# Kernel optimization log

Hardware: AMD Instinct MI355X
Metric: run time of the kernel (lower is better)

The kernel has to match this reference:

```python
import jax, jax.numpy as jnp
import numpy as np
import math

D_MODEL = 1024
D_STATE = 16
D_CONV = 4
EXPAND = 2
D_INNER = EXPAND * D_MODEL
DT_RANK = math.ceil(D_MODEL / 16)
EPS = 1e-5


def setup_inputs() -> dict:
    key = jax.random.key(0)
    ks = jax.random.split(key, 8)
    B, L = 2, 1024
    s = 0.02
    return {
        "hidden_states": jax.random.normal(ks[0], (B, L, D_MODEL), jnp.float32),
        "norm_weight": jnp.ones((D_MODEL,), jnp.float32),
        "in_proj_w": (jax.random.normal(ks[1], (2 * D_INNER, D_MODEL), jnp.float32) * s),
        "conv_w": (jax.random.normal(ks[2], (D_INNER, D_CONV), jnp.float32) * s),
        "conv_b": jnp.zeros((D_INNER,), jnp.float32),
        "x_proj_w": (jax.random.normal(ks[3], (DT_RANK + 2 * D_STATE, D_INNER), jnp.float32) * s),
        "dt_proj_w": (jax.random.normal(ks[4], (D_INNER, DT_RANK), jnp.float32) * s),
        "dt_proj_b": jax.random.uniform(ks[5], (D_INNER,), jnp.float32, -4.0, -2.0),
        "A_log": jnp.log(jnp.broadcast_to(jnp.arange(1, D_STATE + 1, dtype=jnp.float32), (D_INNER, D_STATE))),
        "D": jnp.ones((D_INNER,), jnp.float32),
        "out_proj_w": (jax.random.normal(ks[6], (D_MODEL, D_INNER), jnp.float32) * s),
    }


def _rmsnorm(x, w):
    # Faithful to source: rms = ||x||_2 / sqrt(d); x / (rms + eps) * w
    norm = jnp.linalg.norm(x, axis=-1, keepdims=True)
    rms = norm * (1.0 / math.sqrt(x.shape[-1]))
    return w * (x / (rms + EPS))


def _mamba(h, in_proj_w, conv_w, conv_b, x_proj_w, dt_proj_w, dt_proj_b, A_log, D, out_proj_w):
    B, L, _ = h.shape
    xz = h @ in_proj_w.T                      # (B,L,2*D_INNER)
    x, z = jnp.split(xz, 2, axis=-1)          # each (B,L,D_INNER)

    # causal depthwise conv1d along L, kernel D_CONV
    xpad = jnp.pad(x, ((0, 0), (D_CONV - 1, 0), (0, 0)))
    xc = conv_b
    for k in range(D_CONV):                   # tiny fixed loop over kernel taps
        xc = xc + xpad[:, k:k + L, :] * conv_w[:, k]
    xc = jax.nn.silu(xc)                      # (B,L,D_INNER)

    x_dbl = xc @ x_proj_w.T                   # (B,L,DT_RANK+2N)
    dt, Bm, Cm = jnp.split(x_dbl, [DT_RANK, DT_RANK + D_STATE], axis=-1)
    dt = jax.nn.softplus(dt @ dt_proj_w.T + dt_proj_b)   # (B,L,D_INNER)

    A = -jnp.exp(A_log)                       # (D_INNER,N)
    deltaA = jnp.exp(dt[..., None] * A)                      # (B,L,D_INNER,N)
    deltaBu = (dt * xc)[..., None] * Bm[:, :, None, :]        # (B,L,D_INNER,N)

    def step(hst, inp):
        dA, dBu, Ct = inp
        hst = dA * hst + dBu                  # (B,D_INNER,N)
        y = jnp.einsum('bdn,bn->bd', hst, Ct)
        return hst, y

    h0 = jnp.zeros((B, D_INNER, D_STATE), xc.dtype)
    _, ys = jax.lax.scan(step, h0, (deltaA.swapaxes(0, 1), deltaBu.swapaxes(0, 1), Cm.swapaxes(0, 1)))
    y = ys.swapaxes(0, 1)                     # (B,L,D_INNER)
    y = y + D * xc
    y = y * jax.nn.silu(z)
    return y @ out_proj_w.T                   # (B,L,D_MODEL)


def reference(hidden_states, norm_weight, in_proj_w, conv_w, conv_b, x_proj_w,
              dt_proj_w, dt_proj_b, A_log, D, out_proj_w):
    residual = hidden_states
    h = _rmsnorm(residual, norm_weight)
    out = _mamba(h, in_proj_w, conv_w, conv_b, x_proj_w, dt_proj_w, dt_proj_b,
                 A_log, D, out_proj_w)
    return out, residual
```

## Files before the change

kernel.cpp:

```cpp
#include <hip/hip_runtime.h>

typedef __bf16 bf16x8 __attribute__((ext_vector_type(8)));
typedef float f32x4 __attribute__((ext_vector_type(4)));

__device__ __forceinline__ float b2f(ushort u) {
    union { unsigned int i; float f; } v;
    v.i = ((unsigned int)u) << 16;
    return v.f;
}
__device__ __forceinline__ ushort f2b(float f) {
    union { float f; unsigned int i; } v;
    v.f = f;
    unsigned int x = v.i;
    unsigned int r = (x + 0x7fffu + ((x >> 16) & 1u)) >> 16;
    return (ushort)r;
}
__device__ __forceinline__ float fexp2(float x) {
#if __has_builtin(__builtin_amdgcn_exp2f)
    return __builtin_amdgcn_exp2f(x);
#else
    return exp2f(x);
#endif
}
__device__ __forceinline__ void gload16(const ushort* g, ushort* l) {
    __builtin_amdgcn_global_load_lds(
        (const __attribute__((address_space(1))) unsigned int*)g,
        (__attribute__((address_space(3))) unsigned int*)l, 16, 0, 0);
}
__device__ __forceinline__ bf16x8 ldsfrag(const ushort* s, int row, int cq) {
    int p = cq ^ (row & 7);
    return *(const bf16x8*)(s + row * 64 + p * 8);
}

#define D_MODEL 1024
#define D_INNER 2048
#define D_STATE 16
#define DT_RANK 64
#define NTOK    2048
#define LSEQ    1024
#define NCH     64
#define LC      16
#define KSL     16
#define LOG2E   1.44269504088896f

__global__ __launch_bounds__(256) void prep_kernel(
    const float* __restrict__ hs, const float* __restrict__ w,
    ushort* __restrict__ hout, float* __restrict__ resid,
    const float* __restrict__ inproj, const float* __restrict__ outproj,
    const float* __restrict__ xprojw, const float* __restrict__ dtw,
    ushort* __restrict__ wIn, ushort* __restrict__ wOut,
    ushort* __restrict__ xpw, ushort* __restrict__ dtwb,
    float* __restrict__ xdbl)
{
    int blk = blockIdx.x;
    int tid = threadIdx.x;
    if (blk < NTOK) {
        int t = blk;
        float4 r4 = *(const float4*)(hs + (size_t)t * D_MODEL + tid * 4);
        float s = r4.x * r4.x + r4.y * r4.y + r4.z * r4.z + r4.w * r4.w;
        #pragma unroll
        for (int off = 32; off >= 1; off >>= 1) s += __shfl_xor(s, off);
        __shared__ float red[4];
        int lane = tid & 63, wid = tid >> 6;
        if (lane == 0) red[wid] = s;
        __syncthreads();
        float tot = red[0] + red[1] + red[2] + red[3];
        float inv = 1.0f / (sqrtf(tot) * (1.0f / 32.0f) + 1e-5f);
        float4 w4 = *(const float4*)(w + tid * 4);
        ushort4 o;
        o.x = f2b(w4.x * r4.x * inv);
        o.y = f2b(w4.y * r4.y * inv);
        o.z = f2b(w4.z * r4.z * inv);
        o.w = f2b(w4.w * r4.w * inv);
        *(ushort4*)(hout + (size_t)t * D_MODEL + tid * 4) = o;
        *(float4*)(resid + (size_t)t * D_MODEL + tid * 4) = r4;
    } else if (blk < NTOK + 6464) {
        int i = (blk - NTOK) * 256 + tid;
        const float* src; ushort* dst; int off;
        if (i < 1048576)      { src = inproj;  dst = wIn;  off = i; }
        else if (i < 1572864) { src = outproj; dst = wOut; off = i - 1048576; }
        else if (i < 1622016) { src = xprojw;  dst = xpw;  off = i - 1572864; }
        else if (i < 1654784) { src = dtw;     dst = dtwb; off = i - 1622016; }
        else return;
        float4 v = *(const float4*)(src + (size_t)off * 4);
        ushort4 o;
        o.x = f2b(v.x); o.y = f2b(v.y); o.z = f2b(v.z); o.w = f2b(v.w);
        *(ushort4*)(dst + (size_t)off * 4) = o;
    } else {
        int i = (blk - NTOK - 6464) * 256 + tid;
        if (i < 49152)
            *(float4*)(xdbl + (size_t)i * 4) = (float4){0.f, 0.f, 0.f, 0.f};
    }
}

__global__ __launch_bounds__(256) void gemm_xz_kernel(
    const ushort* __restrict__ Ag, const ushort* __restrict__ Wg,
    ushort* __restrict__ xq, ushort* __restrict__ zq, int K)
{
    __shared__ __align__(16) ushort sA[128 * 64];
    __shared__ __align__(16) ushort sB[128 * 64];
    int tid = threadIdx.x;
    int bm = blockIdx.x, bn = blockIdx.y;
    int wid = tid >> 6, lane = tid & 63;
    int wm = (wid >> 1) * 64, wn = (wid & 1) * 64;
    int l16 = lane & 15, q = lane >> 4;

    f32x4 acc[4][4];
    #pragma unroll
    for (int i = 0; i < 4; i++)
        #pragma unroll
        for (int j = 0; j < 4; j++)
            acc[i][j] = (f32x4){0.f, 0.f, 0.f, 0.f};

    const ushort* Abase = Ag + (size_t)bm * 128 * K;
    const ushort* Wbase = Wg + (size_t)bn * 128 * K;

    int segr = lane >> 3, segc = lane & 7;
    size_t goff[4]; int sseg[4];
    #pragma unroll
    for (int t = 0; t < 4; t++) {
        int s = wid * 4 + t;
        int r = s * 8 + segr;
        int gc = segc ^ (r & 7);
        sseg[t] = s * 512;
        goff[t] = (size_t)r * K + gc * 8;
    }

    for (int k0 = 0; k0 < K; k0 += 64) {
        __syncthreads();
        #pragma unroll
        for (int t = 0; t < 4; t++) {
            gload16(Abase + goff[t] + k0, sA + sseg[t]);
            gload16(Wbase + goff[t] + k0, sB + sseg[t]);
        }
        __syncthreads();
        #pragma unroll
        for (int ks = 0; ks < 2; ks++) {
            int cq = ks * 4 + q;
            bf16x8 af[4], bfr[4];
            #pragma unroll
            for (int i = 0; i < 4; i++)
                af[i] = ldsfrag(sA, wm + i * 16 + l16, cq);
            #pragma unroll
            for (int j = 0; j < 4; j++)
                bfr[j] = ldsfrag(sB, wn + j * 16 + l16, cq);
            #pragma unroll
            for (int i = 0; i < 4; i++)
                #pragma unroll
                for (int j = 0; j < 4; j++)
                    acc[i][j] = __builtin_amdgcn_mfma_f32_16x16x32_bf16(af[i], bfr[j], acc[i][j], 0, 0, 0);
        }
    }

    ushort* dst = (bn < 16) ? xq : zq;
    int row0 = bm * 128 + wm + q * 4;
    int col0 = (bn & 15) * 128 + wn + l16;
    #pragma unroll
    for (int i = 0; i < 4; i++)
        #pragma unroll
        for (int j = 0; j < 4; j++)
            #pragma unroll
            for (int r = 0; r < 4; r++)
                dst[(size_t)(row0 + i * 16 + r) * D_INNER + col0 + j * 16] =
                    f2b(acc[i][j][r]);
}

__global__ __launch_bounds__(256) void gemm64_kernel(
    const ushort* __restrict__ Ag, const ushort* __restrict__ Wg,
    float* __restrict__ Cf, int M, int N, int K)
{
    __shared__ __align__(16) ushort sA[64 * 64];
    __shared__ __align__(16) ushort sB[64 * 64];
    int tid = threadIdx.x;
    int bm = blockIdx.x, bn = blockIdx.y;
    int wid = tid >> 6, lane = tid & 63;
    int wm = wid * 16;
    int l16 = lane & 15, q = lane >> 4;

    f32x4 acc[4];
    #pragma unroll
    for (int j = 0; j < 4; j++) acc[j] = (f32x4){0.f, 0.f, 0.f, 0.f};

    const ushort* Abase = Ag + (size_t)bm * 64 * K;
    const ushort* Wbase = Wg + (size_t)bn * 64 * K;

    int segr = lane >> 3, segc = lane & 7;
    size_t goff[2]; int sseg[2];
    #pragma unroll
    for (int t = 0; t < 2; t++) {
        int s = wid * 2 + t;
        int r = s * 8 + segr;
        int gc = segc ^ (r & 7);
        sseg[t] = s * 512;
        goff[t] = (size_t)r * K + gc * 8;
    }

    for (int k0 = 0; k0 < K; k0 += 64) {
        __syncthreads();
        #pragma unroll
        for (int t = 0; t < 2; t++) {
            gload16(Abase + goff[t] + k0, sA + sseg[t]);
            gload16(Wbase + goff[t] + k0, sB + sseg[t]);
        }
        __syncthreads();
        #pragma unroll
        for (int ks = 0; ks < 2; ks++) {
            int cq = ks * 4 + q;
            bf16x8 af = ldsfrag(sA, wm + l16, cq);
            bf16x8 bfr[4];
            #pragma unroll
            for (int j = 0; j < 4; j++)
                bfr[j] = ldsfrag(sB, j * 16 + l16, cq);
            #pragma unroll
            for (int j = 0; j < 4; j++)
                acc[j] = __builtin_amdgcn_mfma_f32_16x16x32_bf16(af, bfr[j], acc[j], 0, 0, 0);
        }
    }

    int row0 = bm * 64 + wm + q * 4;
    int col0 = bn * 64 + l16;
    #pragma unroll
    for (int j = 0; j < 4; j++)
        #pragma unroll
        for (int r = 0; r < 4; r++)
            Cf[(size_t)(row0 + r) * N + col0 + j * 16] = acc[j][r];
}

__global__ __launch_bounds__(256) void conv_silu_kernel(
    const ushort* __restrict__ xq, const float* __restrict__ cw,
    const float* __restrict__ cb, ushort* __restrict__ xcb)
{
    int idx = blockIdx.x * 256 + threadIdx.x;
    int d = idx & (D_INNER - 1);
    int t = idx >> 11;
    int l = t & (LSEQ - 1), b = t >> 10;
    float4 w4 = *(const float4*)(cw + d * 4);
    float acc = cb[d];
    float wk[4] = {w4.x, w4.y, w4.z, w4.w};
    #pragma unroll
    for (int k = 0; k < 4; k++) {
        int ll = l - 3 + k;
        float xv = (ll >= 0) ? b2f(xq[(((size_t)(b * LSEQ + ll)) << 11) + d]) : 0.f;
        acc += xv * wk[k];
    }
    float sg = acc / (1.f + __expf(-acc));
    xcb[idx] = f2b(sg);
}

__global__ __launch_bounds__(256) void xproj_partial_kernel(
    const ushort* __restrict__ xcb, const ushort* __restrict__ wq,
    float* __restrict__ xdbl)
{
    __shared__ __align__(16) ushort sA[128 * 32];
    __shared__ __align__(16) ushort sB[96 * 32];
    int tid = threadIdx.x;
    int bm = blockIdx.x, sl = blockIdx.y;
    int wid = tid >> 6, lane = tid & 63;
    int wm = wid * 32;
    int l16 = lane & 15, q = lane >> 4;

    f32x4 acc[2][6];
    #pragma unroll
    for (int i = 0; i < 2; i++)
        #pragma unroll
        for (int j = 0; j < 6; j++)
            acc[i][j] = (f32x4){0.f, 0.f, 0.f, 0.f};

    const ushort* Abase = xcb + (size_t)bm * 128 * D_INNER;
    int kbase = sl * (D_INNER / KSL);

    for (int kk = 0; kk < D_INNER / KSL; kk += 32) {
        int k0 = kbase + kk;
        __syncthreads();
        #pragma unroll
        for (int i = tid; i < 512; i += 256) {
            int r = i >> 2, c = (i & 3) << 3;
            *(uint4*)(sA + i * 8) = *(const uint4*)(Abase + (size_t)r * D_INNER + k0 + c);
        }
        for (int i = tid; i < 384; i += 256) {
            int r = i >> 2, c = (i & 3) << 3;
            *(uint4*)(sB + i * 8) = *(const uint4*)(wq + (size_t)r * D_INNER + k0 + c);
        }
        __syncthreads();
        bf16x8 af[2], bfr[6];
        #pragma unroll
        for (int i = 0; i < 2; i++)
            af[i] = *(const bf16x8*)(sA + (wm + i * 16 + l16) * 32 + q * 8);
        #pragma unroll
        for (int j = 0; j < 6; j++)
            bfr[j] = *(const bf16x8*)(sB + (j * 16 + l16) * 32 + q * 8);
        #pragma unroll
        for (int i = 0; i < 2; i++)
            #pragma unroll
            for (int j = 0; j < 6; j++)
                acc[i][j] = __builtin_amdgcn_mfma_f32_16x16x32_bf16(af[i], bfr[j], acc[i][j], 0, 0, 0);
    }

    int row0 = bm * 128 + wm + q * 4;
    #pragma unroll
    for (int i = 0; i < 2; i++)
        #pragma unroll
        for (int j = 0; j < 6; j++)
            #pragma unroll
            for (int r = 0; r < 4; r++)
                atomicAdd(&xdbl[(size_t)(row0 + i * 16 + r) * 96 + j * 16 + l16],
                          acc[i][j][r]);
}

__global__ __launch_bounds__(256) void dt_gemm_kernel(
    const float* __restrict__ xdbl, const ushort* __restrict__ dtwq,
    const float* __restrict__ dtb, ushort* __restrict__ dtout)
{
    __shared__ __align__(16) ushort sA[64 * 72];
    __shared__ __align__(16) ushort sB[64 * 72];
    int tid = threadIdx.x;
    int bm = blockIdx.x, bn = blockIdx.y;
    int wid = tid >> 6, lane = tid & 63;
    int wm = wid * 16;
    int l16 = lane & 15, q = lane >> 4;

    const float* Abase = xdbl + (size_t)bm * 64 * 96;
    const ushort* Bbase = dtwq + (size_t)bn * 64 * DT_RANK;
    #pragma unroll
    for (int i = tid; i < 512; i += 256) {
        int r = i >> 3, c = (i & 7) << 3;
        float4 v0 = *(const float4*)(Abase + (size_t)r * 96 + c);
        float4 v1 = *(const float4*)(Abase + (size_t)r * 96 + c + 4);
        ushort o[8] = {f2b(v0.x), f2b(v0.y), f2b(v0.z), f2b(v0.w),
                       f2b(v1.x), f2b(v1.y), f2b(v1.z), f2b(v1.w)};
        *(uint4*)(sA + r * 72 + c) = *(const uint4*)o;
        *(uint4*)(sB + r * 72 + c) = *(const uint4*)(Bbase + (size_t)r * DT_RANK + c);
    }
    __syncthreads();

    f32x4 acc[4];
    #pragma unroll
    for (int j = 0; j < 4; j++) acc[j] = (f32x4){0.f, 0.f, 0.f, 0.f};

    #pragma unroll
    for (int ks = 0; ks < 2; ks++) {
        bf16x8 af = *(const bf16x8*)(sA + (wm + l16) * 72 + ks * 32 + q * 8);
        bf16x8 bfr[4];
        #pragma unroll
        for (int j = 0; j < 4; j++)
            bfr[j] = *(const bf16x8*)(sB + (j * 16 + l16) * 72 + ks * 32 + q * 8);
        #pragma unroll
        for (int j = 0; j < 4; j++)
            acc[j] = __builtin_amdgcn_mfma_f32_16x16x32_bf16(af, bfr[j], acc[j], 0, 0, 0);
    }

    __syncthreads();
    #pragma unroll
    for (int j = 0; j < 4; j++) {
        float bias = dtb[bn * 64 + j * 16 + l16];
        #pragma unroll
        for (int r = 0; r < 4; r++) {
            float s = acc[j][r] + bias;
            float sp = (s > 20.f) ? s : log1pf(__expf(s));
            sA[(wm + q * 4 + r) * 72 + j * 16 + l16] = f2b(sp);
        }
    }
    __syncthreads();
    int row0 = bm * 64, col0 = bn * 64;
    #pragma unroll
    for (int rep = 0; rep < 2; rep++) {
        int off = rep * 2048 + tid * 8;
        int row = off >> 6, col = off & 63;
        *(uint4*)(dtout + (size_t)(row0 + row) * D_INNER + col0 + col) =
            *(const uint4*)(sA + row * 72 + col);
    }
}

__global__ __launch_bounds__(256) void scan_partA_kernel(
    const ushort* __restrict__ dt, const ushort* __restrict__ xcq,
    const float* __restrict__ xdbl, const float* __restrict__ Alog,
    float2* __restrict__ ch)
{
    __shared__ float sBC[LC][32];
    int bid = blockIdx.x;
    int g = bid & 7;
    int c = (bid >> 3) & (NCH - 1);
    int b = bid >> 9;
    int tid = threadIdx.x;
    int lane = tid & 63, wid = tid >> 6;
    int d = g * 256 + wid * 64 + lane;
    int l0 = c * LC;

    if (tid < LC * 8) {
        int r = tid >> 3, c4 = (tid & 7) * 4;
        *(float4*)&sBC[r][c4] =
            *(const float4*)(xdbl + ((size_t)(b * LSEQ + l0 + r)) * 96 + 64 + c4);
    }
    float A[16];
    #pragma unroll
    for (int k = 0; k < 4; k++)
        *(float4*)&A[k * 4] = *(const float4*)(Alog + d * D_STATE + k * 4);
    #pragma unroll
    for (int n = 0; n < 16; n++) A[n] = -__expf(A[n]) * LOG2E;
    __syncthreads();

    const ushort* dtp = dt  + ((size_t)(b * LSEQ + l0)) * D_INNER + d;
    const ushort* xcp = xcq + ((size_t)(b * LSEQ + l0)) * D_INNER + d;

    float h[16], ap[16];
    #pragma unroll
    for (int n = 0; n < 16; n++) { h[n] = 0.f; ap[n] = 1.f; }

    for (int l = 0; l < LC; l++) {
        float dtv = b2f(dtp[(size_t)l * D_INNER]);
        float xcv = b2f(xcp[(size_t)l * D_INNER]);
        float t = dtv * xcv;
        float Bv[16];
        #pragma unroll
        for (int k = 0; k < 4; k++)
            *(float4*)&Bv[k * 4] = *(const float4*)&sBC[l][k * 4];
        #pragma unroll
        for (int n = 0; n < 16; n++) {
            float a = fexp2(dtv * A[n]);
            h[n] = h[n] * a + t * Bv[n];
            ap[n] *= a;
        }
    }

    float2* outp = ch + (((size_t)(c * 2 + b)) << 15) + (d << 4);
    #pragma unroll
    for (int n = 0; n < 16; n += 2) {
        float4 v = {ap[n], h[n], ap[n + 1], h[n + 1]};
        *(float4*)&outp[n] = v;
    }
}

__global__ __launch_bounds__(256) void scan_partB_kernel(float2* __restrict__ ch)
{
    int kk = blockIdx.x * 256 + threadIdx.x;
    int b = kk >> 15, dn = kk & 32767;
    float run = 0.f;
    #pragma unroll 8
    for (int c = 0; c < NCH; c++) {
        float2* p = ch + (((size_t)(c * 2 + b)) << 15) + dn;
        float2 v = *p;
        p->x = run;
        run = v.x * run + v.y;
    }
}

__global__ __launch_bounds__(256) void scan_partC_kernel(
    const ushort* __restrict__ dt, const ushort* __restrict__ xcq,
    const float* __restrict__ xdbl, const ushort* __restrict__ zq,
    const float* __restrict__ Alog, const float* __restrict__ Dp,
    const float2* __restrict__ ch, ushort* __restrict__ yg)
{
    __shared__ float sBC[LC][32];
    int bid = blockIdx.x;
    int g = bid & 7;
    int c = (bid >> 3) & (NCH - 1);
    int b = bid >> 9;
    int tid = threadIdx.x;
    int lane = tid & 63, wid = tid >> 6;
    int d = g * 256 + wid * 64 + lane;
    int l0 = c * LC;

    if (tid < LC * 8) {
        int r = tid >> 3, c4 = (tid & 7) * 4;
        *(float4*)&sBC[r][c4] =
            *(const float4*)(xdbl + ((size_t)(b * LSEQ + l0 + r)) * 96 + 64 + c4);
    }
    float A[16];
    #pragma unroll
    for (int k = 0; k < 4; k++)
        *(float4*)&A[k * 4] = *(const float4*)(Alog + d * D_STATE + k * 4);
    #pragma unroll
    for (int n = 0; n < 16; n++) A[n] = -__expf(A[n]) * LOG2E;
    float Dd = Dp[d];

    const float2* hip_ = ch + (((size_t)(c * 2 + b)) << 15) + (d << 4);
    float h[16];
    #pragma unroll
    for (int n = 0; n < 16; n += 2) {
        float4 v = *(const float4*)&hip_[n];
        h[n] = v.x; h[n + 1] = v.z;
    }
    __syncthreads();

    const ushort* dtp = dt  + ((size_t)(b * LSEQ + l0)) * D_INNER + d;
    const ushort* xcp = xcq + ((size_t)(b * LSEQ + l0)) * D_INNER + d;
    const ushort* zp  = zq  + ((size_t)(b * LSEQ + l0)) * D_INNER + d;
    ushort* yp = yg + ((size_t)(b * LSEQ + l0)) * D_INNER + d;

    for (int l = 0; l < LC; l++) {
        float dtv = b2f(dtp[(size_t)l * D_INNER]);
        float xcv = b2f(xcp[(size_t)l * D_INNER]);
        float zv  = b2f(zp[(size_t)l * D_INNER]);
        float t = dtv * xcv;
        float Bv[16], Cv[16];
        #pragma unroll
        for (int k = 0; k < 4; k++) {
            *(float4*)&Bv[k * 4] = *(const float4*)&sBC[l][k * 4];
            *(float4*)&Cv[k * 4] = *(const float4*)&sBC[l][16 + k * 4];
        }
        float p0 = 0.f, p1 = 0.f, p2 = 0.f, p3 = 0.f;
        #pragma unroll
        for (int n = 0; n < 16; n += 4) {
            float a0 = fexp2(dtv * A[n]);
            float a1 = fexp2(dtv * A[n + 1]);
            float a2 = fexp2(dtv * A[n + 2]);
            float a3 = fexp2(dtv * A[n + 3]);
            h[n]     = h[n] * a0 + t * Bv[n];
            h[n + 1] = h[n + 1] * a1 + t * Bv[n + 1];
            h[n + 2] = h[n + 2] * a2 + t * Bv[n + 2];
            h[n + 3] = h[n + 3] * a3 + t * Bv[n + 3];
            p0 += h[n] * Cv[n];
            p1 += h[n + 1] * Cv[n + 1];
            p2 += h[n + 2] * Cv[n + 2];
            p3 += h[n + 3] * Cv[n + 3];
        }
        float p = (p0 + p1) + (p2 + p3);
        float y = p + Dd * xcv;
        float sz = zv / (1.f + __expf(-zv));
        yp[(size_t)l * D_INNER] = f2b(y * sz);
    }
}

extern "C" void kernel_launch(void* const* d_in, const int* in_sizes, int n_in,
                              void* d_out, int out_size, void* d_ws, size_t ws_size,
                              hipStream_t stream)
{
    const float* hs      = (const float*)d_in[0];
    const float* norm_w  = (const float*)d_in[1];
    const float* inproj  = (const float*)d_in[2];
    const float* convw   = (const float*)d_in[3];
    const float* convb   = (const float*)d_in[4];
    const float* xprojw  = (const float*)d_in[5];
    const float* dtw     = (const float*)d_in[6];
    const float* dtb     = (const float*)d_in[7];
    const float* alog    = (const float*)d_in[8];
    const float* dvec    = (const float*)d_in[9];
    const float* outproj = (const float*)d_in[10];

    float* out_main  = (float*)d_out;
    float* out_resid = (float*)d_out + (size_t)NTOK * D_MODEL;

    char* ws = (char*)d_ws;
    ushort* xq      = (ushort*)(ws);
    ushort* zq      = (ushort*)(ws +  8388608);
    ushort* dtq     = (ushort*)(ws + 16777216);
    ushort* xcb     = (ushort*)(ws + 25165824);
    float2* ch      = (float2*)(ws + 33554432);
    float*  xdbl    = (float*) (ws + 67108864);
    ushort* wIn     = (ushort*)(ws + 67895296);
    ushort* wOut    = (ushort*)(ws + 76283904);
    ushort* h_bf16  = (ushort*)(ws + 80478208);
    ushort* xpw_b   = (ushort*)(ws + 84672512);
    ushort* dtw_b   = (ushort*)(ws + 85065728);
    ushort* yg_bf16 = (ushort*)(ws + 85327872);

    prep_kernel<<<NTOK + 6464 + 192, 256, 0, stream>>>(
        hs, norm_w, h_bf16, out_resid,
        inproj, outproj, xprojw, dtw, wIn, wOut, xpw_b, dtw_b, xdbl);

    gemm_xz_kernel<<<dim3(NTOK / 128, (2 * D_INNER) / 128), 256, 0, stream>>>(
        h_bf16, wIn, xq, zq, D_MODEL);

    conv_silu_kernel<<<(NTOK * D_INNER) / 256, 256, 0, stream>>>(
        xq, convw, convb, xcb);

    xproj_partial_kernel<<<dim3(NTOK / 128, KSL), 256, 0, stream>>>(
        xcb, xpw_b, xdbl);

    dt_gemm_kernel<<<dim3(NTOK / 64, D_INNER / 64), 256, 0, stream>>>(
        xdbl, dtw_b, dtb, dtq);

    scan_partA_kernel<<<1024, 256, 0, stream>>>(dtq, xcb, xdbl, alog, ch);
    scan_partB_kernel<<<256, 256, 0, stream>>>(ch);
    scan_partC_kernel<<<1024, 256, 0, stream>>>(dtq, xcb, xdbl, zq,
                                                alog, dvec, ch, yg_bf16);

    gemm64_kernel<<<dim3(NTOK / 64, D_MODEL / 64), 256, 0, stream>>>(
        yg_bf16, wOut, out_main, NTOK, D_MODEL, D_INNER);
}
```

Baseline: 254.5 us.

## Retile out-proj GEMM with split-K atomics, vectorize conv, enlarge scan chunks

The output projection moves from 64x64 tiles to 128x128 tiles with a two-way K split that accumulates into a pre-zeroed output using float atomics. The zeroing is added to the prep kernel. Separately, the conv+SiLU kernel is vectorized to eight channels per thread, and the x_proj shared-memory tiles are padded to avoid bank conflicts. The scan chunk count is halved with longer chunks, the chunk-state pass now writes initial states to a separate float buffer, and the scan loops are unrolled. Atomics add non-determinism and extra traffic, and fewer scan blocks lowers parallelism.

```diff
diff --git a/kernel.cpp b/kernel.cpp
--- a/kernel.cpp
+++ b/kernel.cpp
@@ -38,8 +38,8 @@
 #define DT_RANK 64
 #define NTOK    2048
 #define LSEQ    1024
-#define NCH     64
-#define LC      16
+#define NCH     32
+#define LC      32
 #define KSL     16
 #define LOG2E   1.44269504088896f
 
@@ -50,7 +50,7 @@
     const float* __restrict__ xprojw, const float* __restrict__ dtw,
     ushort* __restrict__ wIn, ushort* __restrict__ wOut,
     ushort* __restrict__ xpw, ushort* __restrict__ dtwb,
-    float* __restrict__ xdbl)
+    float* __restrict__ xdbl, float* __restrict__ outz)
 {
     int blk = blockIdx.x;
     int tid = threadIdx.x;
@@ -86,10 +86,14 @@
         ushort4 o;
         o.x = f2b(v.x); o.y = f2b(v.y); o.z = f2b(v.z); o.w = f2b(v.w);
         *(ushort4*)(dst + (size_t)off * 4) = o;
-    } else {
+    } else if (blk < NTOK + 6464 + 192) {
         int i = (blk - NTOK - 6464) * 256 + tid;
         if (i < 49152)
             *(float4*)(xdbl + (size_t)i * 4) = (float4){0.f, 0.f, 0.f, 0.f};
+    } else {
+        int i = (blk - NTOK - 6464 - 192) * 256 + tid;
+        if (i < 524288)
+            *(float4*)(outz + (size_t)i * 4) = (float4){0.f, 0.f, 0.f, 0.f};
     }
 }
 
@@ -165,40 +169,45 @@
                     f2b(acc[i][j][r]);
 }
 
-__global__ __launch_bounds__(256) void gemm64_kernel(
+__global__ __launch_bounds__(256) void gemm_out_kernel(
     const ushort* __restrict__ Ag, const ushort* __restrict__ Wg,
-    float* __restrict__ Cf, int M, int N, int K)
-{
-    __shared__ __align__(16) ushort sA[64 * 64];
-    __shared__ __align__(16) ushort sB[64 * 64];
+    float* __restrict__ Cf)
+{
+    __shared__ __align__(16) ushort sA[128 * 64];
+    __shared__ __align__(16) ushort sB[128 * 64];
+    const int K = D_INNER;
     int tid = threadIdx.x;
-    int bm = blockIdx.x, bn = blockIdx.y;
+    int bm = blockIdx.x, bn = blockIdx.y, bz = blockIdx.z;
     int wid = tid >> 6, lane = tid & 63;
-    int wm = wid * 16;
+    int wm = (wid >> 1) * 64, wn = (wid & 1) * 64;
     int l16 = lane & 15, q = lane >> 4;
 
-    f32x4 acc[4];
-    #pragma unroll
-    for (int j = 0; j < 4; j++) acc[j] = (f32x4){0.f, 0.f, 0.f, 0.f};
-
-    const ushort* Abase = Ag + (size_t)bm * 64 * K;
-    const ushort* Wbase = Wg + (size_t)bn * 64 * K;
+    f32x4 acc[4][4];
+    #pragma unroll
+    for (int i = 0; i < 4; i++)
+        #pragma unroll
+        for (int j = 0; j < 4; j++)
+            acc[i][j] = (f32x4){0.f, 0.f, 0.f, 0.f};
+
+    const ushort* Abase = Ag + (size_t)bm * 128 * K;
+    const ushort* Wbase = Wg + (size_t)bn * 128 * K;
 
     int segr = lane >> 3, segc = lane & 7;
-    size_t goff[2]; int sseg[2];
-    #pragma unroll
-    for (int t = 0; t < 2; t++) {
-        int s = wid * 2 + t;
+    size_t goff[4]; int sseg[4];
+    #pragma unroll
+    for (int t = 0; t < 4; t++) {
+        int s = wid * 4 + t;
         int r = s * 8 + segr;
         int gc = segc ^ (r & 7);
         sseg[t] = s * 512;
         goff[t] = (size_t)r * K + gc * 8;
     }
 
-    for (int k0 = 0; k0 < K; k0 += 64) {
+    int kbeg = bz * (K / 2), kend = kbeg + K / 2;
+    for (int k0 = kbeg; k0 < kend; k0 += 64) {
         __syncthreads();
         #pragma unroll
-        for (int t = 0; t < 2; t++) {
+        for (int t = 0; t < 4; t++) {
             gload16(Abase + goff[t] + k0, sA + sseg[t]);
             gload16(Wbase + goff[t] + k0, sB + sseg[t]);
         }
@@ -206,53 +215,70 @@
         #pragma unroll
         for (int ks = 0; ks < 2; ks++) {
             int cq = ks * 4 + q;
-            bf16x8 af = ldsfrag(sA, wm + l16, cq);
-            bf16x8 bfr[4];
+            bf16x8 af[4], bfr[4];
+            #pragma unroll
+            for (int i = 0; i < 4; i++)
+                af[i] = ldsfrag(sA, wm + i * 16 + l16, cq);
             #pragma unroll
             for (int j = 0; j < 4; j++)
-                bfr[j] = ldsfrag(sB, j * 16 + l16, cq);
-            #pragma unroll
-            for (int j = 0; j < 4; j++)
-                acc[j] = __builtin_amdgcn_mfma_f32_16x16x32_bf16(af, bfr[j], acc[j], 0, 0, 0);
-        }
-    }
-
-    int row0 = bm * 64 + wm + q * 4;
-    int col0 = bn * 64 + l16;
-    #pragma unroll
-    for (int j = 0; j < 4; j++)
-        #pragma unroll
-        for (int r = 0; r < 4; r++)
-            Cf[(size_t)(row0 + r) * N + col0 + j * 16] = acc[j][r];
+                bfr[j] = ldsfrag(sB, wn + j * 16 + l16, cq);
+            #pragma unroll
+            for (int i = 0; i < 4; i++)
+                #pragma unroll
+                for (int j = 0; j < 4; j++)
+                    acc[i][j] = __builtin_amdgcn_mfma_f32_16x16x32_bf16(af[i], bfr[j], acc[i][j], 0, 0, 0);
+        }
+    }
+
+    int row0 = bm * 128 + wm + q * 4;
+    int col0 = bn * 128 + wn + l16;
+    #pragma unroll
+    for (int i = 0; i < 4; i++)
+        #pragma unroll
+        for (int j = 0; j < 4; j++)
+            #pragma unroll
+            for (int r = 0; r < 4; r++)
+                atomicAdd(&Cf[(size_t)(row0 + i * 16 + r) * D_MODEL + col0 + j * 16],
+                          acc[i][j][r]);
 }
 
 __global__ __launch_bounds__(256) void conv_silu_kernel(
     const ushort* __restrict__ xq, const float* __restrict__ cw,
     const float* __restrict__ cb, ushort* __restrict__ xcb)
 {
-    int idx = blockIdx.x * 256 + threadIdx.x;
-    int d = idx & (D_INNER - 1);
-    int t = idx >> 11;
+    int t = blockIdx.x;
+    int d0 = threadIdx.x * 8;
     int l = t & (LSEQ - 1), b = t >> 10;
-    float4 w4 = *(const float4*)(cw + d * 4);
-    float acc = cb[d];
-    float wk[4] = {w4.x, w4.y, w4.z, w4.w};
+
+    ushort v[4][8];
+    bool has[4];
     #pragma unroll
     for (int k = 0; k < 4; k++) {
         int ll = l - 3 + k;
-        float xv = (ll >= 0) ? b2f(xq[(((size_t)(b * LSEQ + ll)) << 11) + d]) : 0.f;
-        acc += xv * wk[k];
-    }
-    float sg = acc / (1.f + __expf(-acc));
-    xcb[idx] = f2b(sg);
+        has[k] = (ll >= 0);
+        if (has[k])
+            *(uint4*)v[k] = *(const uint4*)(xq + (((size_t)(b * LSEQ + ll)) << 11) + d0);
+    }
+    ushort o[8];
+    #pragma unroll
+    for (int j = 0; j < 8; j++) {
+        float4 w4 = *(const float4*)(cw + (size_t)(d0 + j) * 4);
+        float wk[4] = {w4.x, w4.y, w4.z, w4.w};
+        float acc = cb[d0 + j];
+        #pragma unroll
+        for (int k = 0; k < 4; k++)
+            if (has[k]) acc += b2f(v[k][j]) * wk[k];
+        o[j] = f2b(acc / (1.f + __expf(-acc)));
+    }
+    *(uint4*)(xcb + (((size_t)t) << 11) + d0) = *(const uint4*)o;
 }
 
 __global__ __launch_bounds__(256) void xproj_partial_kernel(
     const ushort* __restrict__ xcb, const ushort* __restrict__ wq,
     float* __restrict__ xdbl)
 {
-    __shared__ __align__(16) ushort sA[128 * 32];
-    __shared__ __align__(16) ushort sB[96 * 32];
+    __shared__ __align__(16) ushort sA[128 * 40];
+    __shared__ __align__(16) ushort sB[96 * 40];
     int tid = threadIdx.x;
     int bm = blockIdx.x, sl = blockIdx.y;
     int wid = tid >> 6, lane = tid & 63;
@@ -275,20 +301,20 @@
         #pragma unroll
         for (int i = tid; i < 512; i += 256) {
             int r = i >> 2, c = (i & 3) << 3;
-            *(uint4*)(sA + i * 8) = *(const uint4*)(Abase + (size_t)r * D_INNER + k0 + c);
+            *(uint4*)(sA + r * 40 + c) = *(const uint4*)(Abase + (size_t)r * D_INNER + k0 + c);
         }
         for (int i = tid; i < 384; i += 256) {
             int r = i >> 2, c = (i & 3) << 3;
-            *(uint4*)(sB + i * 8) = *(const uint4*)(wq + (size_t)r * D_INNER + k0 + c);
+            *(uint4*)(sB + r * 40 + c) = *(const uint4*)(wq + (size_t)r * D_INNER + k0 + c);
         }
         __syncthreads();
         bf16x8 af[2], bfr[6];
         #pragma unroll
         for (int i = 0; i < 2; i++)
-            af[i] = *(const bf16x8*)(sA + (wm + i * 16 + l16) * 32 + q * 8);
+            af[i] = *(const bf16x8*)(sA + (wm + i * 16 + l16) * 40 + q * 8);
         #pragma unroll
         for (int j = 0; j < 6; j++)
-            bfr[j] = *(const bf16x8*)(sB + (j * 16 + l16) * 32 + q * 8);
+            bfr[j] = *(const bf16x8*)(sB + (j * 16 + l16) * 40 + q * 8);
         #pragma unroll
         for (int i = 0; i < 2; i++)
             #pragma unroll
@@ -380,13 +406,13 @@
     int bid = blockIdx.x;
     int g = bid & 7;
     int c = (bid >> 3) & (NCH - 1);
-    int b = bid >> 9;
+    int b = bid >> 8;
     int tid = threadIdx.x;
     int lane = tid & 63, wid = tid >> 6;
     int d = g * 256 + wid * 64 + lane;
     int l0 = c * LC;
 
-    if (tid < LC * 8) {
+    {
         int r = tid >> 3, c4 = (tid & 7) * 4;
         *(float4*)&sBC[r][c4] =
             *(const float4*)(xdbl + ((size_t)(b * LSEQ + l0 + r)) * 96 + 64 + c4);
@@ -406,6 +432,7 @@
     #pragma unroll
     for (int n = 0; n < 16; n++) { h[n] = 0.f; ap[n] = 1.f; }
 
+    #pragma unroll 4
     for (int l = 0; l < LC; l++) {
         float dtv = b2f(dtp[(size_t)l * D_INNER]);
         float xcv = b2f(xcp[(size_t)l * D_INNER]);
@@ -430,16 +457,17 @@
     }
 }
 
-__global__ __launch_bounds__(256) void scan_partB_kernel(float2* __restrict__ ch)
+__global__ __launch_bounds__(256) void scan_partB_kernel(
+    const float2* __restrict__ ch, float* __restrict__ hinit)
 {
     int kk = blockIdx.x * 256 + threadIdx.x;
     int b = kk >> 15, dn = kk & 32767;
     float run = 0.f;
     #pragma unroll 8
     for (int c = 0; c < NCH; c++) {
-        float2* p = ch + (((size_t)(c * 2 + b)) << 15) + dn;
-        float2 v = *p;
-        p->x = run;
+        size_t off = (((size_t)(c * 2 + b)) << 15) + dn;
+        float2 v = ch[off];
+        hinit[off] = run;
         run = v.x * run + v.y;
     }
 }
@@ -448,19 +476,19 @@
     const ushort* __restrict__ dt, const ushort* __restrict__ xcq,
     const float* __restrict__ xdbl, const ushort* __restrict__ zq,
     const float* __restrict__ Alog, const float* __restrict__ Dp,
-    const float2* __restrict__ ch, ushort* __restrict__ yg)
+    const float* __restrict__ hinit, ushort* __restrict__ yg)
 {
     __shared__ float sBC[LC][32];
     int bid = blockIdx.x;
     int g = bid & 7;
     int c = (bid >> 3) & (NCH - 1);
-    int b = bid >> 9;
+    int b = bid >> 8;
     int tid = threadIdx.x;
     int lane = tid & 63, wid = tid >> 6;
     int d = g * 256 + wid * 64 + lane;
     int l0 = c * LC;
 
-    if (tid < LC * 8) {
+    {
         int r = tid >> 3, c4 = (tid & 7) * 4;
         *(float4*)&sBC[r][c4] =
             *(const float4*)(xdbl + ((size_t)(b * LSEQ + l0 + r)) * 96 + 64 + c4);
@@ -473,13 +501,11 @@
     for (int n = 0; n < 16; n++) A[n] = -__expf(A[n]) * LOG2E;
     float Dd = Dp[d];
 
-    const float2* hip_ = ch + (((size_t)(c * 2 + b)) << 15) + (d << 4);
+    const float* hp = hinit + (((size_t)(c * 2 + b)) << 15) + (d << 4);
     float h[16];
     #pragma unroll
-    for (int n = 0; n < 16; n += 2) {
-        float4 v = *(const float4*)&hip_[n];
-        h[n] = v.x; h[n + 1] = v.z;
-    }
+    for (int n = 0; n < 16; n += 4)
+        *(float4*)&h[n] = *(const float4*)(hp + n);
     __syncthreads();
 
     const ushort* dtp = dt  + ((size_t)(b * LSEQ + l0)) * D_INNER + d;
@@ -487,6 +513,7 @@
     const ushort* zp  = zq  + ((size_t)(b * LSEQ + l0)) * D_INNER + d;
     ushort* yp = yg + ((size_t)(b * LSEQ + l0)) * D_INNER + d;
 
+    #pragma unroll 4
     for (int l = 0; l < LC; l++) {
         float dtv = b2f(dtp[(size_t)l * D_INNER]);
         float xcv = b2f(xcp[(size_t)l * D_INNER]);
@@ -546,6 +573,7 @@
     ushort* dtq     = (ushort*)(ws + 16777216);
     ushort* xcb     = (ushort*)(ws + 25165824);
     float2* ch      = (float2*)(ws + 33554432);
+    float*  hinit   = (float*) (ws + 50331648);
     float*  xdbl    = (float*) (ws + 67108864);
     ushort* wIn     = (ushort*)(ws + 67895296);
     ushort* wOut    = (ushort*)(ws + 76283904);
@@ -554,15 +582,14 @@
     ushort* dtw_b   = (ushort*)(ws + 85065728);
     ushort* yg_bf16 = (ushort*)(ws + 85327872);
 
-    prep_kernel<<<NTOK + 6464 + 192, 256, 0, stream>>>(
+    prep_kernel<<<NTOK + 6464 + 192 + 2048, 256, 0, stream>>>(
         hs, norm_w, h_bf16, out_resid,
-        inproj, outproj, xprojw, dtw, wIn, wOut, xpw_b, dtw_b, xdbl);
+        inproj, outproj, xprojw, dtw, wIn, wOut, xpw_b, dtw_b, xdbl, out_main);
 
     gemm_xz_kernel<<<dim3(NTOK / 128, (2 * D_INNER) / 128), 256, 0, stream>>>(
         h_bf16, wIn, xq, zq, D_MODEL);
 
-    conv_silu_kernel<<<(NTOK * D_INNER) / 256, 256, 0, stream>>>(
-        xq, convw, convb, xcb);
+    conv_silu_kernel<<<NTOK, 256, 0, stream>>>(xq, convw, convb, xcb);
 
     xproj_partial_kernel<<<dim3(NTOK / 128, KSL), 256, 0, stream>>>(
         xcb, xpw_b, xdbl);
@@ -570,11 +597,11 @@
     dt_gemm_kernel<<<dim3(NTOK / 64, D_INNER / 64), 256, 0, stream>>>(
         xdbl, dtw_b, dtb, dtq);
 
-    scan_partA_kernel<<<1024, 256, 0, stream>>>(dtq, xcb, xdbl, alog, ch);
-    scan_partB_kernel<<<256, 256, 0, stream>>>(ch);
-    scan_partC_kernel<<<1024, 256, 0, stream>>>(dtq, xcb, xdbl, zq,
-                                                alog, dvec, ch, yg_bf16);
-
-    gemm64_kernel<<<dim3(NTOK / 64, D_MODEL / 64), 256, 0, stream>>>(
-        yg_bf16, wOut, out_main, NTOK, D_MODEL, D_INNER);
-}
+    scan_partA_kernel<<<512, 256, 0, stream>>>(dtq, xcb, xdbl, alog, ch);
+    scan_partB_kernel<<<256, 256, 0, stream>>>(ch, hinit);
+    scan_partC_kernel<<<512, 256, 0, stream>>>(dtq, xcb, xdbl, zq,
+                                               alog, dvec, hinit, yg_bf16);
+
+    gemm_out_kernel<<<dim3(NTOK / 128, D_MODEL / 128, 2), 256, 0, stream>>>(
+        yg_bf16, wOut, out_main);
+}
```

New measurement: 277.8 us. 1.09x slower.
